# Kernel optimization log

Measured on AMD Instinct MI355X. Metric: run time of the kernel, lower is better.

## Reference

```python
import jax, jax.numpy as jnp
import numpy as np

D = 65536
N_T, N_G, N_L = 256, 256, 1024


def setup_inputs() -> dict:
    key = jax.random.key(0)
    k1, k2, k3 = jax.random.split(key, 3)
    return {
        "out_student_global": jax.random.normal(k1, (N_G, D), dtype=jnp.float32),
        "out_student_local": jax.random.normal(k2, (N_L, D), dtype=jnp.float32),
        "out_teacher": jax.random.normal(k3, (N_T, D), dtype=jnp.float32),
        "center": jnp.zeros((1, D), dtype=jnp.float32),
        "temp_student": jnp.array([0.1], dtype=jnp.float32),
        "temp_teacher": jnp.array([0.04], dtype=jnp.float32),
        "cent_rate_m": jnp.array([0.9], dtype=jnp.float32),
    }


def reference(out_student_global, out_student_local, out_teacher, center,
              temp_student, temp_teacher, cent_rate_m):
    # Student log-probabilities (log_softmax of each part, then concat --
    # identical to concat-then-log_softmax since softmax is row-wise).
    log_prob_s_g = jax.nn.log_softmax(out_student_global / temp_student, axis=-1)
    log_prob_s_l = jax.nn.log_softmax(out_student_local / temp_student, axis=-1)
    log_prob_s = jnp.concatenate([log_prob_s_g, log_prob_s_l], axis=0)  # [Ns, D]
    # Teacher probabilities with centering.
    prob_t = jax.nn.softmax((out_teacher - center) / temp_teacher, axis=-1)  # [Nt, D]
    # All pairwise cross-entropies in one matmul: ce[i, j] = -sum_d p_t[i,d] * log q_s[j,d]
    ce = -jnp.einsum('td,sd->ts', prob_t, log_prob_s)  # [Nt, Ns]
    n_t, n_s = ce.shape
    diag_mask = jnp.arange(n_t)[:, None] == jnp.arange(n_s)[None, :]  # skip i == j
    total_loss = jnp.sum(jnp.where(diag_mask, jnp.zeros((), ce.dtype), ce))
    n_loss_terms = n_t * n_s - min(n_t, n_s)  # static count of off-diagonal pairs
    return total_loss / n_loss_terms
```

## Files before the change

### kernel.cpp

```cpp
#include <hip/hip_runtime.h>
#include <math.h>

#define D 65536
#define NT 256
#define NG 256
#define NL 1024
#define NS 1280
#define CT 32
#define TILE_W 2048
#define RG 40
#define ROWS_PER_BLK 32
#define KC_SPLIT 4

typedef float vfloat4 __attribute__((ext_vector_type(4)));


__global__ __launch_bounds__(256) void kA(const float* __restrict__ sg,
                                          const float* __restrict__ sl,
                                          const float* __restrict__ tempS,
                                          float* __restrict__ Sxs,
                                          float2* __restrict__ stats) {
    const int tid  = threadIdx.x;
    const int lane = tid & 63;
    const int w    = tid >> 6;
    const int ct   = blockIdx.x;
    const int gy   = blockIdx.y;
    const int c0   = ct * TILE_W;
    const float invTs = 1.0f / tempS[0];

    __shared__ float lds_sx[4][TILE_W];

    float sx[32];
    #pragma unroll
    for (int j = 0; j < 32; ++j) sx[j] = 0.0f;

    for (int i = 0; i < 8; ++i) {
        const int r = gy * ROWS_PER_BLK + i * 4 + w;
        const bool is_local = (r >= NG);
        const float* row = is_local ? (sl + (size_t)(r - NG) * D)
                                    : (sg + (size_t)r * D);
        float u[32];
        #pragma unroll
        for (int ch = 0; ch < 8; ++ch) {
            const vfloat4* p = (const vfloat4*)(row + c0 + ch * 256) + lane;
            vfloat4 v = is_local ? __builtin_nontemporal_load(p) : *p;
            u[ch*4+0] = v.x * invTs;
            u[ch*4+1] = v.y * invTs;
            u[ch*4+2] = v.z * invTs;
            u[ch*4+3] = v.w * invTs;
        }
        float m = u[0];
        #pragma unroll
        for (int j = 1; j < 32; ++j) m = fmaxf(m, u[j]);
        #pragma unroll
        for (int off = 32; off; off >>= 1) m = fmaxf(m, __shfl_xor(m, off, 64));
        float z = 0.0f;
        #pragma unroll
        for (int j = 0; j < 32; ++j) z += __expf(u[j] - m);
        #pragma unroll
        for (int off = 32; off; off >>= 1) z += __shfl_xor(z, off, 64);
        if (lane == 0) stats[ct * NS + r] = make_float2(m, z);
        #pragma unroll
        for (int j = 0; j < 32; ++j) sx[j] += u[j];
    }

    #pragma unroll
    for (int ch = 0; ch < 8; ++ch) {
        #pragma unroll
        for (int j = 0; j < 4; ++j)
            lds_sx[w][ch*256 + lane*4 + j] = sx[ch*4 + j];
    }
    __syncthreads();
    #pragma unroll
    for (int k = 0; k < 8; ++k) {
        const int idx = tid * 8 + k;
        const float v = lds_sx[0][idx] + lds_sx[1][idx] + lds_sx[2][idx] + lds_sx[3][idx];
        atomicAdd(&Sxs[c0 + idx], v);
    }
}

__global__ __launch_bounds__(256) void kC(const float* __restrict__ tch,
                                          const float* __restrict__ sg,
                                          const float* __restrict__ center,
                                          const float* __restrict__ Sxs,
                                          const float* __restrict__ tempS,
                                          const float* __restrict__ tempT,
                                          float4* __restrict__ tup) {
    const int t   = blockIdx.x >> 2;
    const int q   = blockIdx.x & 3;
    const int tid = threadIdx.x;
    const float invTt = 1.0f / tempT[0];
    const float invTs = 1.0f / tempS[0];

    const float4* xt = (const float4*)(tch + (size_t)t * D);
    const float4* xg = (const float4*)(sg  + (size_t)t * D);
    const float4* c4 = (const float4*)center;
    const float4* s4 = (const float4*)Sxs;

    float m = -INFINITY, Z = 0.0f, A = 0.0f, Dg = 0.0f;
    const int base = q * 4096;
    for (int it = 0; it < 16; ++it) {
        const int idx = base + it * 256 + tid;
        const float4 x = xt[idx];
        const float4 c = c4[idx];
        const float4 g = xg[idx];
        const float4 s = s4[idx];
        const float ys[4] = {(x.x-c.x)*invTt, (x.y-c.y)*invTt, (x.z-c.z)*invTt, (x.w-c.w)*invTt};
        const float gs[4] = {g.x*invTs, g.y*invTs, g.z*invTs, g.w*invTs};
        const float ss[4] = {s.x, s.y, s.z, s.w};
        #pragma unroll
        for (int j = 0; j < 4; ++j) {
            const float y  = ys[j];
            const float mn = fmaxf(m, y);
            const float sc = __expf(m - mn);
            const float f  = __expf(y - mn);
            Z  = Z  * sc + f;
            A  = A  * sc + f * ss[j];
            Dg = Dg * sc + f * gs[j];
            m  = mn;
        }
    }
    #pragma unroll
    for (int off = 32; off; off >>= 1) {
        const float m2 = __shfl_xor(m,  off, 64);
        const float Z2 = __shfl_xor(Z,  off, 64);
        const float A2 = __shfl_xor(A,  off, 64);
        const float G2 = __shfl_xor(Dg, off, 64);
        const float mn = fmaxf(m, m2);
        const float s1 = __expf(m  - mn);
        const float s2 = __expf(m2 - mn);
        Z  = Z  * s1 + Z2 * s2;
        A  = A  * s1 + A2 * s2;
        Dg = Dg * s1 + G2 * s2;
        m  = mn;
    }
    __shared__ float4 lds[4];
    const int w = tid >> 6, lane = tid & 63;
    if (lane == 0) lds[w] = make_float4(m, Z, A, Dg);
    __syncthreads();
    if (tid == 0) {
        float4 r = lds[0];
        for (int k = 1; k < 4; ++k) {
            const float4 p = lds[k];
            const float mn = fmaxf(r.x, p.x);
            const float s1 = __expf(r.x - mn);
            const float s2 = __expf(p.x - mn);
            r = make_float4(mn, r.y*s1 + p.y*s2, r.z*s1 + p.z*s2, r.w*s1 + p.w*s2);
        }
        tup[blockIdx.x] = r;
    }
}

__global__ __launch_bounds__(256) void kD(const float2* __restrict__ stats,
                                          const float4* __restrict__ tup,
                                          float* __restrict__ out) {
    const int tid = threadIdx.x;
    float accC = 0.0f, accCg = 0.0f;
    for (int r = tid; r < NS; r += 256) {
        float m = -INFINITY, Z = 0.0f;
        for (int ct = 0; ct < CT; ++ct) {
            const float2 p = stats[ct * NS + r];
            const float mn = fmaxf(m, p.x);
            Z = Z * __expf(m - mn) + p.y * __expf(p.x - mn);
            m = mn;
        }
        const float l = m + logf(Z);
        accC += l;
        if (r < NG) accCg += l;
    }
    float termS = 0.0f;
    if (tid < NT) {
        float4 r = tup[KC_SPLIT * tid];
        for (int k = 1; k < KC_SPLIT; ++k) {
            const float4 p = tup[KC_SPLIT * tid + k];
            const float mn = fmaxf(r.x, p.x);
            const float s1 = __expf(r.x - mn);
            const float s2 = __expf(p.x - mn);
            r = make_float4(mn, r.y*s1 + p.y*s2, r.z*s1 + p.z*s2, r.w*s1 + p.w*s2);
        }
        termS = (r.z - r.w) / r.y;
    }
    #pragma unroll
    for (int off = 32; off; off >>= 1) {
        accC  += __shfl_xor(accC,  off, 64);
        accCg += __shfl_xor(accCg, off, 64);
        termS += __shfl_xor(termS, off, 64);
    }
    __shared__ float l1[4], l2[4], l3[4];
    const int w = tid >> 6, lane = tid & 63;
    if (lane == 0) { l1[w] = accC; l2[w] = accCg; l3[w] = termS; }
    __syncthreads();
    if (tid == 0) {
        float C = 0.0f, Cg = 0.0f, S = 0.0f;
        for (int k = 0; k < 4; ++k) { C += l1[k]; Cg += l2[k]; S += l3[k]; }
        out[0] = (256.0f * C - Cg - S) * (1.0f / 327424.0f);
    }
}

extern "C" void kernel_launch(void* const* d_in, const int* in_sizes, int n_in,
                              void* d_out, int out_size, void* d_ws, size_t ws_size,
                              hipStream_t stream) {
    const float* sg     = (const float*)d_in[0];
    const float* sl     = (const float*)d_in[1];
    const float* tch    = (const float*)d_in[2];
    const float* center = (const float*)d_in[3];
    const float* tempS  = (const float*)d_in[4];
    const float* tempT  = (const float*)d_in[5];

    float* ws = (float*)d_ws;
    float*  Sxs   = ws;
    float2* stats = (float2*)(ws + D);
    float4* tup   = (float4*)(ws + D + CT * NS * 2);

    hipMemsetAsync(Sxs, 0, D * sizeof(float), stream);
    kA<<<dim3(CT, RG), 256, 0, stream>>>(sg, sl, tempS, Sxs, stats);
    kC<<<NT * KC_SPLIT, 256, 0, stream>>>(tch, sg, center, Sxs, tempS, tempT, tup);
    kD<<<1, 256, 0, stream>>>(stats, tup, (float*)d_out);
}
```

Baseline: 524.2 us.

## Replace column-sum atomics with partial buffers and streamline softmax loops

kA now computes its row max and sum with an online, per-vector update on float4 values instead of buffering 32 values and running two passes. When the workspace is large enough, it writes per-row-group column partial sums to a buffer, and a new kernel kB reduces them, replacing the memset and atomics. kC's split doubles to 8 and its online softmax updates once per float4 instead of once per element. The change also drops the nontemporal loads on the local rows, and the extra kB pass costs more launches and memory traffic.

```diff
diff --git a/kernel.cpp b/kernel.cpp
--- a/kernel.cpp
+++ b/kernel.cpp
@@ -10,16 +10,22 @@
 #define TILE_W 2048
 #define RG 40
 #define ROWS_PER_BLK 32
-#define KC_SPLIT 4
+#define KC_SPLIT 8
 
 typedef float vfloat4 __attribute__((ext_vector_type(4)));
 
+
+__device__ __forceinline__ float max4(vfloat4 v) {
+    return fmaxf(fmaxf(v.x, v.y), fmaxf(v.z, v.w));
+}
 
 __global__ __launch_bounds__(256) void kA(const float* __restrict__ sg,
                                           const float* __restrict__ sl,
                                           const float* __restrict__ tempS,
                                           float* __restrict__ Sxs,
-                                          float2* __restrict__ stats) {
+                                          float* __restrict__ partial,
+                                          float2* __restrict__ stats,
+                                          int use_atomic) {
     const int tid  = threadIdx.x;
     const int lane = tid & 63;
     const int w    = tid >> 6;
@@ -30,53 +36,70 @@
 
     __shared__ float lds_sx[4][TILE_W];
 
-    float sx[32];
-    #pragma unroll
-    for (int j = 0; j < 32; ++j) sx[j] = 0.0f;
+    vfloat4 sx[8];
+    #pragma unroll
+    for (int j = 0; j < 8; ++j) sx[j] = (vfloat4)0.0f;
 
     for (int i = 0; i < 8; ++i) {
         const int r = gy * ROWS_PER_BLK + i * 4 + w;
-        const bool is_local = (r >= NG);
-        const float* row = is_local ? (sl + (size_t)(r - NG) * D)
-                                    : (sg + (size_t)r * D);
-        float u[32];
+        const float* row = (r >= NG) ? (sl + (size_t)(r - NG) * D)
+                                     : (sg + (size_t)r * D);
+        const vfloat4* p = (const vfloat4*)(row + c0) + lane;
+
+        float m = -INFINITY, z = 0.0f;
         #pragma unroll
         for (int ch = 0; ch < 8; ++ch) {
-            const vfloat4* p = (const vfloat4*)(row + c0 + ch * 256) + lane;
-            vfloat4 v = is_local ? __builtin_nontemporal_load(p) : *p;
-            u[ch*4+0] = v.x * invTs;
-            u[ch*4+1] = v.y * invTs;
-            u[ch*4+2] = v.z * invTs;
-            u[ch*4+3] = v.w * invTs;
-        }
-        float m = u[0];
+            vfloat4 v = p[ch * 64];
+            vfloat4 u = v * invTs;
+            sx[ch] += u;
+            const float mn = fmaxf(m, max4(u));
+            const float f0 = __expf(u.x - mn);
+            const float f1 = __expf(u.y - mn);
+            const float f2 = __expf(u.z - mn);
+            const float f3 = __expf(u.w - mn);
+            z = z * __expf(m - mn) + ((f0 + f1) + (f2 + f3));
+            m = mn;
+        }
         #pragma unroll
-        for (int j = 1; j < 32; ++j) m = fmaxf(m, u[j]);
-        #pragma unroll
-        for (int off = 32; off; off >>= 1) m = fmaxf(m, __shfl_xor(m, off, 64));
-        float z = 0.0f;
-        #pragma unroll
-        for (int j = 0; j < 32; ++j) z += __expf(u[j] - m);
-        #pragma unroll
-        for (int off = 32; off; off >>= 1) z += __shfl_xor(z, off, 64);
+        for (int off = 32; off; off >>= 1) {
+            const float m2 = __shfl_xor(m, off, 64);
+            const float z2 = __shfl_xor(z, off, 64);
+            const float mn = fmaxf(m, m2);
+            z = z * __expf(m - mn) + z2 * __expf(m2 - mn);
+            m = mn;
+        }
         if (lane == 0) stats[ct * NS + r] = make_float2(m, z);
-        #pragma unroll
-        for (int j = 0; j < 32; ++j) sx[j] += u[j];
-    }
-
-    #pragma unroll
-    for (int ch = 0; ch < 8; ++ch) {
-        #pragma unroll
-        for (int j = 0; j < 4; ++j)
-            lds_sx[w][ch*256 + lane*4 + j] = sx[ch*4 + j];
-    }
+    }
+
+    #pragma unroll
+    for (int ch = 0; ch < 8; ++ch)
+        ((vfloat4*)&lds_sx[w][ch * 256])[lane] = sx[ch];
     __syncthreads();
-    #pragma unroll
-    for (int k = 0; k < 8; ++k) {
-        const int idx = tid * 8 + k;
-        const float v = lds_sx[0][idx] + lds_sx[1][idx] + lds_sx[2][idx] + lds_sx[3][idx];
-        atomicAdd(&Sxs[c0 + idx], v);
-    }
+
+    #pragma unroll
+    for (int k = 0; k < 2; ++k) {
+        const int i4 = k * 256 + tid;
+        vfloat4 v = ((vfloat4*)lds_sx[0])[i4] + ((vfloat4*)lds_sx[1])[i4]
+                  + ((vfloat4*)lds_sx[2])[i4] + ((vfloat4*)lds_sx[3])[i4];
+        if (use_atomic) {
+            const int c = c0 + i4 * 4;
+            atomicAdd(&Sxs[c + 0], v.x);
+            atomicAdd(&Sxs[c + 1], v.y);
+            atomicAdd(&Sxs[c + 2], v.z);
+            atomicAdd(&Sxs[c + 3], v.w);
+        } else {
+            ((vfloat4*)(partial + (size_t)gy * D + c0))[i4] = v;
+        }
+    }
+}
+
+__global__ __launch_bounds__(256) void kB(const float* __restrict__ partial,
+                                          float* __restrict__ Sxs) {
+    const int col = blockIdx.x * 256 + threadIdx.x;
+    float s = 0.0f;
+    #pragma unroll 8
+    for (int g = 0; g < RG; ++g) s += partial[(size_t)g * D + col];
+    Sxs[col] = s;
 }
 
 __global__ __launch_bounds__(256) void kC(const float* __restrict__ tch,
@@ -86,8 +109,8 @@
                                           const float* __restrict__ tempS,
                                           const float* __restrict__ tempT,
                                           float4* __restrict__ tup) {
-    const int t   = blockIdx.x >> 2;
-    const int q   = blockIdx.x & 3;
+    const int t   = blockIdx.x / KC_SPLIT;
+    const int q   = blockIdx.x % KC_SPLIT;
     const int tid = threadIdx.x;
     const float invTt = 1.0f / tempT[0];
     const float invTs = 1.0f / tempS[0];
@@ -98,27 +121,23 @@
     const float4* s4 = (const float4*)Sxs;
 
     float m = -INFINITY, Z = 0.0f, A = 0.0f, Dg = 0.0f;
-    const int base = q * 4096;
-    for (int it = 0; it < 16; ++it) {
+    const int base = q * (D / 4 / KC_SPLIT);
+    for (int it = 0; it < (D / 4 / KC_SPLIT) / 256; ++it) {
         const int idx = base + it * 256 + tid;
         const float4 x = xt[idx];
         const float4 c = c4[idx];
         const float4 g = xg[idx];
         const float4 s = s4[idx];
-        const float ys[4] = {(x.x-c.x)*invTt, (x.y-c.y)*invTt, (x.z-c.z)*invTt, (x.w-c.w)*invTt};
-        const float gs[4] = {g.x*invTs, g.y*invTs, g.z*invTs, g.w*invTs};
-        const float ss[4] = {s.x, s.y, s.z, s.w};
-        #pragma unroll
-        for (int j = 0; j < 4; ++j) {
-            const float y  = ys[j];
-            const float mn = fmaxf(m, y);
-            const float sc = __expf(m - mn);
-            const float f  = __expf(y - mn);
-            Z  = Z  * sc + f;
-            A  = A  * sc + f * ss[j];
-            Dg = Dg * sc + f * gs[j];
-            m  = mn;
-        }
+        const float y0 = (x.x - c.x) * invTt, y1 = (x.y - c.y) * invTt;
+        const float y2 = (x.z - c.z) * invTt, y3 = (x.w - c.w) * invTt;
+        const float mn = fmaxf(m, fmaxf(fmaxf(y0, y1), fmaxf(y2, y3)));
+        const float sc = __expf(m - mn);
+        const float f0 = __expf(y0 - mn), f1 = __expf(y1 - mn);
+        const float f2 = __expf(y2 - mn), f3 = __expf(y3 - mn);
+        Z  = Z  * sc + ((f0 + f1) + (f2 + f3));
+        A  = A  * sc + ((f0 * s.x + f1 * s.y) + (f2 * s.z + f3 * s.w));
+        Dg = Dg * sc + ((f0 * g.x + f1 * g.y) + (f2 * g.z + f3 * g.w)) * invTs;
+        m  = mn;
     }
     #pragma unroll
     for (int off = 32; off; off >>= 1) {
@@ -208,12 +227,19 @@
     const float* tempT  = (const float*)d_in[5];
 
     float* ws = (float*)d_ws;
-    float*  Sxs   = ws;
-    float2* stats = (float2*)(ws + D);
-    float4* tup   = (float4*)(ws + D + CT * NS * 2);
-
-    hipMemsetAsync(Sxs, 0, D * sizeof(float), stream);
-    kA<<<dim3(CT, RG), 256, 0, stream>>>(sg, sl, tempS, Sxs, stats);
+    float*  Sxs     = ws;
+    float2* stats   = (float2*)(ws + D);
+    float4* tup     = (float4*)(ws + D + CT * NS * 2);
+    float*  partial = ws + D + CT * NS * 2 + NT * KC_SPLIT * 4;
+
+    const size_t needed = (size_t)(D + CT * NS * 2 + NT * KC_SPLIT * 4 + RG * D) * sizeof(float);
+    const int use_atomic = (ws_size < needed) ? 1 : 0;
+
+    if (use_atomic)
+        hipMemsetAsync(Sxs, 0, D * sizeof(float), stream);
+    kA<<<dim3(CT, RG), 256, 0, stream>>>(sg, sl, tempS, Sxs, partial, stats, use_atomic);
+    if (!use_atomic)
+        kB<<<D / 256, 256, 0, stream>>>(partial, Sxs);
     kC<<<NT * KC_SPLIT, 256, 0, stream>>>(tch, sg, center, Sxs, tempS, tempT, tup);
     kD<<<1, 256, 0, stream>>>(stats, tup, (float*)d_out);
 }
```

Result: faster. 500.6 us (-4.5%).
